# Kernel optimization log

Hardware: AMD Instinct MI355X
Metric: run time of the kernel (lower is better)

The kernel has to match this reference:

```python
import jax, jax.numpy as jnp
import numpy as np

PAD_IDX = 0
NEG = -1e9


def gru_step(h, x, Wih, Whh, bih, bhh):
    # PyTorch GRU cell. Wih: [3H, In], Whh: [3H, H]
    gi = x @ Wih.T + bih
    gh = h @ Whh.T + bhh
    H = h.shape[-1]
    i_r, i_z, i_n = gi[..., :H], gi[..., H:2 * H], gi[..., 2 * H:]
    h_r, h_z, h_n = gh[..., :H], gh[..., H:2 * H], gh[..., 2 * H:]
    r = jax.nn.sigmoid(i_r + h_r)
    z = jax.nn.sigmoid(i_z + h_z)
    n = jnp.tanh(i_n + r * h_n)
    return (1.0 - z) * n + z * h


def setup_inputs() -> dict:
    key = jax.random.key(0)
    V, E, H, C = 256, 512, 1024, 128
    NM, NT, NP = 8, 12, 8
    B, S, T = 256, 96, 40
    ks = iter(jax.random.split(key, 40))

    def p(shape, scale=0.05):
        return (jax.random.normal(next(ks), shape, dtype=jnp.float32) * scale)

    enc_emb = p((V, E)).at[PAD_IDX].set(0.0)
    dec_emb = p((V, E)).at[PAD_IDX].set(0.0)
    inp = dict(
        src=jax.random.randint(next(ks), (B, S), 0, V, dtype=jnp.int32),
        tgt=jax.random.randint(next(ks), (B, T), 0, V, dtype=jnp.int32),
        mode_idx=jax.random.randint(next(ks), (B,), 0, NM, dtype=jnp.int32),
        tense_idx=jax.random.randint(next(ks), (B,), 0, NT, dtype=jnp.int32),
        person_idx=jax.random.randint(next(ks), (B,), 0, NP, dtype=jnp.int32),
        enc_emb=enc_emb,
        enc_Wih_f=p((3 * H, E)), enc_Whh_f=p((3 * H, H)),
        enc_bih_f=p((3 * H,)), enc_bhh_f=p((3 * H,)),
        enc_Wih_b=p((3 * H, E)), enc_Whh_b=p((3 * H, H)),
        enc_bih_b=p((3 * H,)), enc_bhh_b=p((3 * H,)),
        Wa=p((H, 3 * H)),           # attn: Linear(2H + H -> H), no bias
        va=p((1, H)),               # v: Linear(H -> 1), no bias
        dec_emb=dec_emb,
        dec_Wih=p((3 * H, E + 2 * H)), dec_Whh=p((3 * H, H)),
        dec_bih=p((3 * H,)), dec_bhh=p((3 * H,)),
        Wfc=p((V, H + 2 * H + E)), bfc=p((V,)),
        mode_E=p((NM, C)).at[0].set(0.0),
        tense_E=p((NT, C)).at[0].set(0.0),
        person_E=p((NP, C)).at[0].set(0.0),
        Wbr=p((H, 2 * H + 3 * C)), bbr=p((H,)),
    )
    return inp


def reference(src, tgt, mode_idx, tense_idx, person_idx,
              enc_emb, enc_Wih_f, enc_Whh_f, enc_bih_f, enc_bhh_f,
              enc_Wih_b, enc_Whh_b, enc_bih_b, enc_bhh_b,
              Wa, va, dec_emb, dec_Wih, dec_Whh, dec_bih, dec_bhh,
              Wfc, bfc, mode_E, tense_E, person_E, Wbr, bbr):
    B, S = src.shape
    T = tgt.shape[1]
    H = dec_Whh.shape[1]

    # ---- Encoder: bidirectional GRU ----
    x = enc_emb[src]                       # [B,S,E]
    xs = jnp.swapaxes(x, 0, 1)             # [S,B,E]
    h0 = jnp.zeros((B, H), dtype=x.dtype)

    def fstep(h, xt):
        h2 = gru_step(h, xt, enc_Wih_f, enc_Whh_f, enc_bih_f, enc_bhh_f)
        return h2, h2

    def bstep(h, xt):
        h2 = gru_step(h, xt, enc_Wih_b, enc_Whh_b, enc_bih_b, enc_bhh_b)
        return h2, h2

    hf, outs_f = jax.lax.scan(fstep, h0, xs)
    hb, outs_b = jax.lax.scan(bstep, h0, xs[::-1])
    outs_b = outs_b[::-1]
    enc_out = jnp.swapaxes(jnp.concatenate([outs_f, outs_b], axis=-1), 0, 1)  # [B,S,2H]
    enc_hidden = jnp.concatenate([hf, hb], axis=-1)                           # [B,2H]

    # ---- Bridge init of decoder hidden ----
    cond = jnp.concatenate([enc_hidden, mode_E[mode_idx], tense_E[tense_idx],
                            person_E[person_idx]], axis=-1)
    dec_h0 = jnp.tanh(cond @ Wbr.T + bbr)  # [B,H]

    # ---- Attention precompute (linear is separable over the concat) ----
    Wa_h, Wa_e = Wa[:, :H], Wa[:, H:]
    enc_proj = jnp.einsum('bsd,hd->bsh', enc_out, Wa_e)  # [B,S,H]
    src_mask = (src != PAD_IDX)

    # ---- Decoder greedy loop (eval: no teacher forcing) ----
    def step(carry, _):
        h, tok = carry
        energy = jnp.tanh(h @ Wa_h.T[None] if False else jnp.tanh(0))  # placeholder
        energy = jnp.tanh((h @ Wa_h.T)[:, None, :] + enc_proj)          # [B,S,H]
        scores = jnp.einsum('bsh,h->bs', energy, va[0])
        scores = jnp.where(src_mask, scores, NEG)
        w = jax.nn.softmax(scores, axis=-1)
        ctx = jnp.einsum('bs,bsd->bd', w, enc_out)                      # [B,2H]
        emb = dec_emb[tok]                                              # [B,E]
        rnn_in = jnp.concatenate([emb, ctx], axis=-1)
        h2 = gru_step(h, rnn_in, dec_Wih, dec_Whh, dec_bih, dec_bhh)
        pred = jnp.concatenate([h2, ctx, emb], axis=-1) @ Wfc.T + bfc   # [B,V]
        tok2 = jnp.argmax(pred, axis=-1).astype(tok.dtype)
        return (h2, tok2), pred

    (_, _), preds = jax.lax.scan(step, (dec_h0, tgt[:, 0]), None, length=T - 1)
    return jnp.swapaxes(preds, 0, 1)  # [B, T-1, V]
```

## Files before the change

kernel.cpp:

```cpp
#include <hip/hip_runtime.h>
#include <hip/hip_fp16.h>
#include <cstdint>
#include <cstddef>

#define B_  256
#define S_  96
#define T_  40
#define V_  256
#define E_  512
#define H_  1024
#define C_  128

typedef __attribute__((ext_vector_type(8))) short s8v;
typedef __attribute__((ext_vector_type(4))) float f4v;
typedef _Float16 h8v __attribute__((ext_vector_type(8)));

__device__ __forceinline__ float sigmoidf_(float x) { return 1.0f / (1.0f + expf(-x)); }

__device__ __forceinline__ uint32_t cvtpk_bf16(float a, float b) {
  uint32_t r;
  asm("v_cvt_pk_bf16_f32 %0, %1, %2" : "=v"(r) : "v"(a), "v"(b));
  return r;
}

union U4 { uint32_t u[4]; s8v v; };

__device__ __forceinline__ void split8(const float4 a, const float4 b, s8v& hi, s8v& lo) {
  U4 H, L;
  H.u[0] = cvtpk_bf16(a.x, a.y);
  H.u[1] = cvtpk_bf16(a.z, a.w);
  H.u[2] = cvtpk_bf16(b.x, b.y);
  H.u[3] = cvtpk_bf16(b.z, b.w);
  const float r0 = a.x - __uint_as_float(H.u[0] << 16);
  const float r1 = a.y - __uint_as_float(H.u[0] & 0xffff0000u);
  const float r2 = a.z - __uint_as_float(H.u[1] << 16);
  const float r3 = a.w - __uint_as_float(H.u[1] & 0xffff0000u);
  const float r4 = b.x - __uint_as_float(H.u[2] << 16);
  const float r5 = b.y - __uint_as_float(H.u[2] & 0xffff0000u);
  const float r6 = b.z - __uint_as_float(H.u[3] << 16);
  const float r7 = b.w - __uint_as_float(H.u[3] & 0xffff0000u);
  L.u[0] = cvtpk_bf16(r0, r1);
  L.u[1] = cvtpk_bf16(r2, r3);
  L.u[2] = cvtpk_bf16(r4, r5);
  L.u[3] = cvtpk_bf16(r6, r7);
  hi = H.v; lo = L.v;
}

__global__ void wsplit_k(const float* __restrict__ Wf, const float* __restrict__ Wb,
                         short* __restrict__ hi, short* __restrict__ lo, int n)
{
  const int i = blockIdx.x * 256 + threadIdx.x;
  const float w = (i < n) ? Wf[i] : Wb[i - n];
  const uint32_t h = cvtpk_bf16(w, w) & 0xffffu;
  const float wh = __uint_as_float(h << 16);
  const uint32_t l = cvtpk_bf16(w - wh, w - wh) & 0xffffu;
  hi[i] = (short)h;
  lo[i] = (short)l;
}

__global__ void split_plane_k(const float* __restrict__ src, int ld_src, int col0,
                              short* __restrict__ hi, short* __restrict__ lo,
                              int ld_p, int pcol0, int total, int cols)
{
  const int i = blockIdx.x * 256 + threadIdx.x;
  if (i >= total) return;
  const int r = i / cols, c = i % cols;
  const float w = src[(size_t)r * ld_src + col0 + c];
  const uint32_t h = cvtpk_bf16(w, w) & 0xffffu;
  const float wh = __uint_as_float(h << 16);
  const uint32_t l = cvtpk_bf16(w - wh, w - wh) & 0xffffu;
  const size_t o = (size_t)r * ld_p + pcol0 + c;
  hi[o] = (short)h;
  lo[o] = (short)l;
}

__global__ void split_plane_h_k(const float* __restrict__ src, int ld_src, int col0,
                                __half* __restrict__ hi, __half* __restrict__ lo,
                                int ld_p, int total, int cols)
{
  const int i = blockIdx.x * 256 + threadIdx.x;
  if (i >= total) return;
  const int r = i / cols, c = i % cols;
  const float w = src[(size_t)r * ld_src + col0 + c];
  const __half h = __float2half(w);
  const __half l = __float2half(w - __half2float(h));
  const size_t o = (size_t)r * ld_p + c;
  hi[o] = h;
  lo[o] = l;
}

struct EM {
  const int* gidx; int goff0, goff1;
  const float* Gt0; const float* Gt1;
  const float* h0; const float* h1; int ldh;
  const short* whi; const short* wlo;
  const float* bih0; const float* bih1;
  const float* bhh0; const float* bhh1;
  float* d0; float* d1;
  __half* e0; __half* e1; int lde;
};

__global__ __launch_bounds__(256)
void enc_mfma_k(EM g)
{
  const int fid = (blockIdx.x & 7) * 64 + (blockIdx.x >> 3);
  const int m0 = (fid & 3) * 64;
  const int r2 = fid >> 2;
  const int dir = r2 & 1;
  const int q0 = (r2 >> 1) * 16;

  __shared__ int rows[64];
  const int tid = threadIdx.x;
  if (tid < 64)
    rows[tid] = g.gidx[(size_t)(m0 + tid) * S_ + (dir ? g.goff1 : g.goff0)];
  __syncthreads();

  const int w = tid >> 6, lane = tid & 63;
  const int arow = m0 + 16 * w + (lane & 15);
  const int kc = (lane >> 4) << 3;
  const float* hsrc = dir ? g.h1 : g.h0;
  const short* whi = g.whi + (size_t)dir * (3u * H_ * H_);
  const short* wlo = g.wlo + (size_t)dir * (3u * H_ * H_);
  const float* ap = hsrc + (size_t)arow * g.ldh;
  const int wrow = q0 + (lane & 15);

  f4v acc[3];
  acc[0] = f4v{0.f, 0.f, 0.f, 0.f};
  acc[1] = f4v{0.f, 0.f, 0.f, 0.f};
  acc[2] = f4v{0.f, 0.f, 0.f, 0.f};

  float4 a0 = *(const float4*)(ap + kc);
  float4 a1 = *(const float4*)(ap + kc + 4);
  s8v bh[3], bl[3];
#pragma unroll
  for (int g3 = 0; g3 < 3; ++g3) {
    const size_t wb = (size_t)(g3 * H_ + wrow) * H_ + kc;
    bh[g3] = *(const s8v*)(whi + wb);
    bl[g3] = *(const s8v*)(wlo + wb);
  }

  for (int kb = 0; kb < 1024; kb += 32) {
    float4 na0, na1;
    s8v nbh[3], nbl[3];
    if (kb + 32 < 1024) {
      na0 = *(const float4*)(ap + kb + 32 + kc);
      na1 = *(const float4*)(ap + kb + 32 + kc + 4);
#pragma unroll
      for (int g3 = 0; g3 < 3; ++g3) {
        const size_t wb = (size_t)(g3 * H_ + wrow) * H_ + kb + 32 + kc;
        nbh[g3] = *(const s8v*)(whi + wb);
        nbl[g3] = *(const s8v*)(wlo + wb);
      }
    }
    s8v ah, al;
    split8(a0, a1, ah, al);
#pragma unroll
    for (int g3 = 0; g3 < 3; ++g3) {
      acc[g3] = __builtin_amdgcn_mfma_f32_16x16x32_bf16(ah, bh[g3], acc[g3], 0, 0, 0);
      acc[g3] = __builtin_amdgcn_mfma_f32_16x16x32_bf16(al, bh[g3], acc[g3], 0, 0, 0);
      acc[g3] = __builtin_amdgcn_mfma_f32_16x16x32_bf16(ah, bl[g3], acc[g3], 0, 0, 0);
    }
    a0 = na0; a1 = na1;
#pragma unroll
    for (int g3 = 0; g3 < 3; ++g3) { bh[g3] = nbh[g3]; bl[g3] = nbl[g3]; }
  }

  const float* bih = dir ? g.bih1 : g.bih0;
  const float* bhh = dir ? g.bhh1 : g.bhh0;
  const float* Gt = dir ? g.Gt1 : g.Gt0;
  float* dst = dir ? g.d1 : g.d0;
  __half* edst = dir ? g.e1 : g.e0;
  const int col = q0 + (lane & 15);
  const float bir = bih[col], biz = bih[H_ + col], bin = bih[2 * H_ + col];
  const float bhr = bhh[col], bhz = bhh[H_ + col], bhn = bhh[2 * H_ + col];
#pragma unroll
  for (int r = 0; r < 4; ++r) {
    const int b = m0 + 16 * w + (lane >> 4) * 4 + r;
    const float* Gr = Gt + (size_t)rows[b - m0] * (3 * H_);
    const float hold = hsrc[(size_t)b * g.ldh + col];
    const float rr = sigmoidf_(acc[0][r] + Gr[col] + bir + bhr);
    const float zz = sigmoidf_(acc[1][r] + Gr[H_ + col] + biz + bhz);
    const float nn = tanhf(Gr[2 * H_ + col] + bin + rr * (acc[2][r] + bhn));
    const float hv = (1.f - zz) * nn + zz * hold;
    dst[(size_t)b * H_ + col] = hv;
    edst[(size_t)b * g.lde + col] = __float2half(hv);
  }
}

struct DM {
  const float* predin;
  const float* h;
  const int* tok;
  const float* Gd;
  const short* whi; const short* wlo;
  const float* bih; const float* bhh;
  float* d;
  float* predout;
};

__global__ __launch_bounds__(768)
void dec_mfma_k(DM g)
{
  const int fid = (blockIdx.x & 7) * 32 + (blockIdx.x >> 3);
  const int m0 = (fid & 3) * 64;
  const int q0 = (fid >> 2) * 16;
  const int tid = threadIdx.x;
  const int w = tid >> 6, lane = tid & 63;
  const int mg = w & 3;
  const int gate = w >> 2;

  __shared__ short sA[2][2][64][40];
  __shared__ float eacc[4][64][16];

  const int srow = tid >> 2;
  const int skq = (tid & 3) << 3;
  const float* actx = g.predin + (size_t)(m0 + srow) * 3584 + 1024;
  const float* ahid = g.h + (size_t)(m0 + srow) * H_;
  auto loadA8 = [&](int kk, float4& x0, float4& x1) {
    const float* p = (kk < 2048) ? (actx + kk) : (ahid + kk - 2048);
    x0 = *(const float4*)p;
    x1 = *(const float4*)(p + 4);
  };

  const int kc = (lane >> 4) << 3;
  const int wrow = gate * H_ + q0 + (lane & 15);
  const short* whp = g.whi + (size_t)wrow * 3072 + kc;
  const short* wlp = g.wlo + (size_t)wrow * 3072 + kc;

  f4v acc0 = f4v{0.f, 0.f, 0.f, 0.f};
  f4v acc1 = acc0;

  float4 sx0, sx1;
  if (tid < 256) loadA8(skq, sx0, sx1);
  s8v bh = *(const s8v*)whp;
  s8v bl = *(const s8v*)wlp;
  if (tid < 256) {
    s8v ah, al;
    split8(sx0, sx1, ah, al);
    *(s8v*)&sA[0][0][srow][skq] = ah;
    *(s8v*)&sA[0][1][srow][skq] = al;
  }
  __syncthreads();

  const int arowl = mg * 16 + (lane & 15);
  for (int ch = 0; ch < 96; ++ch) {
    const int buf = ch & 1;
    float4 nx0, nx1;
    if (tid < 256 && ch + 1 < 96) loadA8((ch + 1) * 32 + skq, nx0, nx1);
    s8v nbh, nbl;
    if (ch + 1 < 96) {
      nbh = *(const s8v*)(whp + (ch + 1) * 32);
      nbl = *(const s8v*)(wlp + (ch + 1) * 32);
    }
    const s8v ah = *(const s8v*)&sA[buf][0][arowl][kc];
    const s8v al = *(const s8v*)&sA[buf][1][arowl][kc];
    if (gate < 2) {
      acc0 = __builtin_amdgcn_mfma_f32_16x16x32_bf16(ah, bh, acc0, 0, 0, 0);
      acc0 = __builtin_amdgcn_mfma_f32_16x16x32_bf16(al, bh, acc0, 0, 0, 0);
      acc0 = __builtin_amdgcn_mfma_f32_16x16x32_bf16(ah, bl, acc0, 0, 0, 0);
    } else if (ch < 64) {
      acc0 = __builtin_amdgcn_mfma_f32_16x16x32_bf16(ah, bh, acc0, 0, 0, 0);
      acc0 = __builtin_amdgcn_mfma_f32_16x16x32_bf16(al, bh, acc0, 0, 0, 0);
      acc0 = __builtin_amdgcn_mfma_f32_16x16x32_bf16(ah, bl, acc0, 0, 0, 0);
    } else {
      acc1 = __builtin_amdgcn_mfma_f32_16x16x32_bf16(ah, bh, acc1, 0, 0, 0);
      acc1 = __builtin_amdgcn_mfma_f32_16x16x32_bf16(al, bh, acc1, 0, 0, 0);
      acc1 = __builtin_amdgcn_mfma_f32_16x16x32_bf16(ah, bl, acc1, 0, 0, 0);
    }
    if (tid < 256 && ch + 1 < 96) {
      s8v ah2, al2;
      split8(nx0, nx1, ah2, al2);
      *(s8v*)&sA[buf ^ 1][0][srow][skq] = ah2;
      *(s8v*)&sA[buf ^ 1][1][srow][skq] = al2;
    }
    bh = nbh; bl = nbl;
    __syncthreads();
  }

#pragma unroll
  for (int r = 0; r < 4; ++r) {
    const int lr = mg * 16 + (lane >> 4) * 4 + r;
    if (gate < 2) {
      eacc[gate][lr][lane & 15] = acc0[r];
    } else {
      eacc[2][lr][lane & 15] = acc0[r];
      eacc[3][lr][lane & 15] = acc1[r];
    }
  }
  __syncthreads();

  for (int o = tid; o < 1024; o += 768) {
    const int lr = o >> 4, lc = o & 15;
    const int b = m0 + lr, col = q0 + lc;
    const float* Gr = g.Gd + (size_t)g.tok[b] * (3 * H_);
    const float hold = g.h[(size_t)b * H_ + col];
    const float rr = sigmoidf_(eacc[0][lr][lc] + Gr[col] + g.bih[col] + g.bhh[col]);
    const float zz = sigmoidf_(eacc[1][lr][lc] + Gr[H_ + col] + g.bih[H_ + col] + g.bhh[H_ + col]);
    const float nn = tanhf(eacc[2][lr][lc] + Gr[2 * H_ + col] + g.bih[2 * H_ + col]
                           + rr * (eacc[3][lr][lc] + g.bhh[2 * H_ + col]));
    const float hv = (1.f - zz) * nn + zz * hold;
    g.d[(size_t)b * H_ + col] = hv;
    g.predout[(size_t)b * 3584 + col] = hv;
  }
}

__global__ __launch_bounds__(256)
void proj_mfma_k(const __half* __restrict__ enc, const __half* __restrict__ whi,
                 const __half* __restrict__ wlo, __half* __restrict__ proj)
{
  const int fid = (blockIdx.x & 7) * 768 + (blockIdx.x >> 3);
  const int w = threadIdx.x >> 6, lane = threadIdx.x & 63;
  const int wg = fid * 4 + w;
  const int ng = wg / 1536;
  const int mt = wg % 1536;
  const int n0 = ng * 64;
  const int kc = (lane >> 4) << 3;
  const __half* ap = enc + (size_t)(mt * 16 + (lane & 15)) * 2048 + kc;
  const __half* bhp = whi + (size_t)(n0 + (lane & 15)) * 2048 + kc;
  const __half* blp = wlo + (size_t)(n0 + (lane & 15)) * 2048 + kc;

  f4v acc[4];
#pragma unroll
  for (int j = 0; j < 4; ++j) acc[j] = f4v{0.f, 0.f, 0.f, 0.f};

  h8v a = *(const h8v*)ap;
  h8v bh[4], bl[4];
#pragma unroll
  for (int j = 0; j < 4; ++j) {
    bh[j] = *(const h8v*)(bhp + (size_t)j * 16 * 2048);
    bl[j] = *(const h8v*)(blp + (size_t)j * 16 * 2048);
  }

  for (int kb = 0; kb < 2048; kb += 32) {
    h8v na, nbh[4], nbl[4];
    if (kb + 32 < 2048) {
      na = *(const h8v*)(ap + kb + 32);
#pragma unroll
      for (int j = 0; j < 4; ++j) {
        nbh[j] = *(const h8v*)(bhp + (size_t)j * 16 * 2048 + kb + 32);
        nbl[j] = *(const h8v*)(blp + (size_t)j * 16 * 2048 + kb + 32);
      }
    }
#pragma unroll
    for (int j = 0; j < 4; ++j) {
      acc[j] = __builtin_amdgcn_mfma_f32_16x16x32_f16(a, bh[j], acc[j], 0, 0, 0);
      acc[j] = __builtin_amdgcn_mfma_f32_16x16x32_f16(a, bl[j], acc[j], 0, 0, 0);
    }
    a = na;
#pragma unroll
    for (int j = 0; j < 4; ++j) { bh[j] = nbh[j]; bl[j] = nbl[j]; }
  }

#pragma unroll
  for (int j = 0; j < 4; ++j)
#pragma unroll
    for (int r = 0; r < 4; ++r) {
      const int row = mt * 16 + (lane >> 4) * 4 + r;
      proj[(size_t)row * H_ + n0 + j * 16 + (lane & 15)] = __float2half(acc[j][r]);
    }
}

__global__ __launch_bounds__(256)
void prqa_mfma_k(const float* __restrict__ predin,
                 const short* __restrict__ fhi, const short* __restrict__ flo,
                 const float* __restrict__ bfc,
                 const float* __restrict__ hnew,
                 const short* __restrict__ qhi, const short* __restrict__ qlo,
                 float* __restrict__ out_t, float* __restrict__ qout)
{
  const int bid = blockIdx.x, tid = threadIdx.x;
  const int w = tid >> 6, lane = tid & 63;
  const int kc = (lane >> 4) << 3;
  if (bid < 256) {
    const int m0 = (bid >> 4) << 4, n0 = (bid & 15) << 4;
    const float* ap = predin + (size_t)(m0 + (lane & 15)) * 3584 + w * 896;
    const short* bhp = fhi + (size_t)(n0 + (lane & 15)) * 3584 + w * 896;
    const short* blp = flo + (size_t)(n0 + (lane & 15)) * 3584 + w * 896;
    f4v acc = f4v{0.f, 0.f, 0.f, 0.f};
    float4 a0 = *(const float4*)(ap + kc), a1 = *(const float4*)(ap + kc + 4);
    s8v bh = *(const s8v*)(bhp + kc), bl = *(const s8v*)(blp + kc);
    for (int kb = 0; kb < 896; kb += 32) {
      float4 na0, na1; s8v nbh, nbl;
      if (kb + 32 < 896) {
        na0 = *(const float4*)(ap + kb + 32 + kc);
        na1 = *(const float4*)(ap + kb + 32 + kc + 4);
        nbh = *(const s8v*)(bhp + kb + 32 + kc);
        nbl = *(const s8v*)(blp + kb + 32 + kc);
      }
      s8v ah, al;
      split8(a0, a1, ah, al);
      acc = __builtin_amdgcn_mfma_f32_16x16x32_bf16(ah, bh, acc, 0, 0, 0);
      acc = __builtin_amdgcn_mfma_f32_16x16x32_bf16(al, bh, acc, 0, 0, 0);
      acc = __builtin_amdgcn_mfma_f32_16x16x32_bf16(ah, bl, acc, 0, 0, 0);
      a0 = na0; a1 = na1; bh = nbh; bl = nbl;
    }
    __shared__ float red[4][64][4];
#pragma unroll
    for (int r = 0; r < 4; ++r) red[w][lane][r] = acc[r];
    __syncthreads();
    const int row = tid >> 4, col = tid & 15;
    const int sl = col + ((row >> 2) << 4), reg = row & 3;
    const float s = red[0][sl][reg] + red[1][sl][reg] + red[2][sl][reg] + red[3][sl][reg];
    out_t[(size_t)(m0 + row) * ((T_ - 1) * V_) + n0 + col] = s + bfc[n0 + col];
  } else {
    const int tt = (bid - 256) * 4 + w;
    const int m0 = (tt >> 6) << 4, n0 = (tt & 63) << 4;
    const float* ap = hnew + (size_t)(m0 + (lane & 15)) * H_;
    const short* bhp = qhi + (size_t)(n0 + (lane & 15)) * H_;
    const short* blp = qlo + (size_t)(n0 + (lane & 15)) * H_;
    f4v acc = f4v{0.f, 0.f, 0.f, 0.f};
    float4 a0 = *(const float4*)(ap + kc), a1 = *(const float4*)(ap + kc + 4);
    s8v bh = *(const s8v*)(bhp + kc), bl = *(const s8v*)(blp + kc);
    for (int kb = 0; kb < 1024; kb += 32) {
      float4 na0, na1; s8v nbh, nbl;
      if (kb + 32 < 1024) {
        na0 = *(const float4*)(ap + kb + 32 + kc);
        na1 = *(const float4*)(ap + kb + 32 + kc + 4);
        nbh = *(const s8v*)(bhp + kb + 32 + kc);
        nbl = *(const s8v*)(blp + kb + 32 + kc);
      }
      s8v ah, al;
      split8(a0, a1, ah, al);
      acc = __builtin_amdgcn_mfma_f32_16x16x32_bf16(ah, bh, acc, 0, 0, 0);
      acc = __builtin_amdgcn_mfma_f32_16x16x32_bf16(al, bh, acc, 0, 0, 0);
      acc = __builtin_amdgcn_mfma_f32_16x16x32_bf16(ah, bl, acc, 0, 0, 0);
      a0 = na0; a1 = na1; bh = nbh; bl = nbl;
    }
#pragma unroll
    for (int r = 0; r < 4; ++r)
      qout[(size_t)(m0 + (lane >> 4) * 4 + r) * H_ + n0 + (lane & 15)] = acc[r];
  }
}

__global__ __launch_bounds__(512)
void attn1_k(const float* __restrict__ out, const int* __restrict__ tgt,
             const float* __restrict__ q, const __half* __restrict__ proj,
             const float* __restrict__ va, const int* __restrict__ src,
             const float* __restrict__ dec_emb,
             float* __restrict__ predin, float* __restrict__ wts,
             int* __restrict__ tokbuf, int t)
{
  const int b = blockIdx.x, tid = threadIdx.x;
  const int lane = tid & 63, wv = tid >> 6;
  __shared__ float sm[128];
  __shared__ float tr[128];
  __shared__ float rv[4];
  __shared__ int ri[4];
  __shared__ int tok_s;
  if (t == 0) {
    if (tid == 0) tok_s = tgt[(size_t)b * T_];
  } else {
    if (tid < 256) {
      float av = out[((size_t)b * (T_ - 1) + (t - 1)) * V_ + tid];
      int ai = tid;
      for (int off = 32; off; off >>= 1) {
        const float ov = __shfl_down(av, off);
        const int   oi = __shfl_down(ai, off);
        if (ov > av) { av = ov; ai = oi; }
      }
      if (lane == 0) { rv[wv] = av; ri[wv] = ai; }
    }
    __syncthreads();
    if (tid == 0) {
      float bv = rv[0]; int bi = ri[0];
      for (int w2 = 1; w2 < 4; ++w2) if (rv[w2] > bv) { bv = rv[w2]; bi = ri[w2]; }
      tok_s = bi;
    }
  }
  __syncthreads();
  const int tok = tok_s;
  if (tid == 0) tokbuf[b] = tok;
  predin[(size_t)b * 3584 + 3072 + tid] = dec_emb[(size_t)tok * E_ + tid];
  const float* qb = q + (size_t)b * H_;
  for (int s = wv * 12; s < wv * 12 + 12; ++s) {
    const __half* pb = proj + ((size_t)b * S_ + s) * H_;
    float part = 0.f;
#pragma unroll
    for (int j = 0; j < 8; ++j) {
      const int h = lane * 2 + j * 128;
      const __half2 p2 = *(const __half2*)(pb + h);
      const float2 q2 = *(const float2*)(qb + h);
      const float2 v2 = *(const float2*)(va + h);
      part += v2.x * tanhf(q2.x + __half2float(p2.x));
      part += v2.y * tanhf(q2.y + __half2float(p2.y));
    }
    for (int off = 32; off; off >>= 1) part += __shfl_down(part, off);
    if (lane == 0)
      sm[s] = (src[(size_t)b * S_ + s] == 0) ? -1.0e9f : part;
  }
  __syncthreads();
  if (tid < 128) tr[tid] = (tid < S_) ? sm[tid] : -3.0e38f;
  __syncthreads();
  for (int s2 = 64; s2 > 0; s2 >>= 1) { if (tid < s2) tr[tid] = fmaxf(tr[tid], tr[tid + s2]); __syncthreads(); }
  const float mx = tr[0];
  __syncthreads();
  if (tid < 128) tr[tid] = (tid < S_) ? expf(sm[tid] - mx) : 0.f;
  __syncthreads();
  for (int s2 = 64; s2 > 0; s2 >>= 1) { if (tid < s2) tr[tid] += tr[tid + s2]; __syncthreads(); }
  const float inv = 1.0f / tr[0];
  __syncthreads();
  if (tid < S_) wts[(size_t)b * S_ + tid] = expf(sm[tid] - mx) * inv;
}

__global__ __launch_bounds__(256)
void ctx_k(const float* __restrict__ wts, const __half* __restrict__ enc,
           float* __restrict__ predin)
{
  const int b = blockIdx.y, tid = threadIdx.x;
  __shared__ float sw[S_];
  if (tid < S_) sw[tid] = wts[(size_t)b * S_ + tid];
  __syncthreads();
  const int d = blockIdx.x * 512 + tid * 2;
  const __half* eb = enc + (size_t)b * S_ * (2 * H_) + d;
  float c0 = 0.f, c1 = 0.f;
  for (int s0 = 0; s0 < S_; s0 += 8) {
    __half2 v[8];
#pragma unroll
    for (int i = 0; i < 8; ++i) v[i] = *(const __half2*)(eb + (size_t)(s0 + i) * (2 * H_));
#pragma unroll
    for (int i = 0; i < 8; ++i) {
      const float w = sw[s0 + i];
      c0 += w * __half2float(v[i].x);
      c1 += w * __half2float(v[i].y);
    }
  }
  *(float2*)(predin + (size_t)b * 3584 + H_ + d) = make_float2(c0, c1);
}

struct GB {
  const float* A; int lda;
  const __half* Ah;
  const float* W; int ldw;
  const float* bias;
  float* C; int ldc;
  __half* Ch;
  int M, N, K, act;
  const float *hf, *hb; int ldh;
  const float *mE, *tE, *pE;
  const int *mi, *ti, *pi;
};

template<int AMODE, int CMODE>
__global__ __launch_bounds__(256)
void gemm_k(GB g0, GB g1)
{
  GB g = blockIdx.z ? g1 : g0;
  const int m0 = blockIdx.y * 64, n0 = blockIdx.x * 64;
  if (m0 >= g.M || n0 >= g.N) return;
  __shared__ float As[32][68];
  __shared__ float Ws[32][68];
  const int tid = threadIdx.x, tx = tid & 15, ty = tid >> 4;
  const int lm = tid >> 3, lk = (tid & 7) << 2;
  float acc[4][4] = {};
  float4 av[2], wv[2], av2[2], wv2[2];

  auto load_tile = [&](int k0, float4 (&AV)[2], float4 (&WV)[2]) {
#pragma unroll
    for (int i = 0; i < 2; ++i) {
      const int row = lm + i * 32;
      const int kk = k0 + lk;
      if (AMODE == 0) {
        AV[i] = *(const float4*)(g.A + (size_t)(m0 + row) * g.lda + kk);
      } else if (AMODE == 4) {
        const __half* ap = g.Ah + (size_t)(m0 + row) * g.lda + kk;
        const __half2 h0 = *(const __half2*)ap;
        const __half2 h1 = *(const __half2*)(ap + 2);
        AV[i] = make_float4(__half2float(h0.x), __half2float(h0.y),
                            __half2float(h1.x), __half2float(h1.y));
      } else {
        const int mg = m0 + row; const float* sp; size_t o;
        if (kk < 1024)      { sp = g.hf; o = (size_t)mg * g.ldh + kk; }
        else if (kk < 2048) { sp = g.hb; o = (size_t)mg * g.ldh + kk - 1024; }
        else if (kk < 2176) { sp = g.mE; o = (size_t)g.mi[mg] * C_ + kk - 2048; }
        else if (kk < 2304) { sp = g.tE; o = (size_t)g.ti[mg] * C_ + kk - 2176; }
        else                { sp = g.pE; o = (size_t)g.pi[mg] * C_ + kk - 2304; }
        AV[i] = *(const float4*)(sp + o);
      }
      WV[i] = *(const float4*)(g.W + (size_t)(n0 + row) * g.ldw + kk);
    }
  };

  load_tile(0, av, wv);
  for (int k0 = 0; k0 < g.K; k0 += 32) {
    __syncthreads();
#pragma unroll
    for (int i = 0; i < 2; ++i) {
      const int row = lm + i * 32;
      As[lk + 0][row] = av[i].x; As[lk + 1][row] = av[i].y;
      As[lk + 2][row] = av[i].z; As[lk + 3][row] = av[i].w;
      Ws[lk + 0][row] = wv[i].x; Ws[lk + 1][row] = wv[i].y;
      Ws[lk + 2][row] = wv[i].z; Ws[lk + 3][row] = wv[i].w;
    }
    __syncthreads();
    if (k0 + 32 < g.K) load_tile(k0 + 32, av2, wv2);
#pragma unroll
    for (int k = 0; k < 32; ++k) {
      const float4 a4 = *(const float4*)&As[k][ty << 2];
      const float4 b4 = *(const float4*)&Ws[k][tx << 2];
      acc[0][0] += a4.x * b4.x; acc[0][1] += a4.x * b4.y; acc[0][2] += a4.x * b4.z; acc[0][3] += a4.x * b4.w;
      acc[1][0] += a4.y * b4.x; acc[1][1] += a4.y * b4.y; acc[1][2] += a4.y * b4.z; acc[1][3] += a4.y * b4.w;
      acc[2][0] += a4.z * b4.x; acc[2][1] += a4.z * b4.y; acc[2][2] += a4.z * b4.z; acc[2][3] += a4.z * b4.w;
      acc[3][0] += a4.w * b4.x; acc[3][1] += a4.w * b4.y; acc[3][2] += a4.w * b4.z; acc[3][3] += a4.w * b4.w;
    }
#pragma unroll
    for (int i = 0; i < 2; ++i) { av[i] = av2[i]; wv[i] = wv2[i]; }
  }
  const int n = n0 + (tx << 2);
  float4 bb = make_float4(0.f, 0.f, 0.f, 0.f);
  if (g.bias) bb = *(const float4*)(g.bias + n);
#pragma unroll
  for (int i = 0; i < 4; ++i) {
    const int m = m0 + (ty << 2) + i;
    float4 v = make_float4(acc[i][0] + bb.x, acc[i][1] + bb.y, acc[i][2] + bb.z, acc[i][3] + bb.w);
    if (CMODE == 0) {
      if (g.act) { v.x = tanhf(v.x); v.y = tanhf(v.y); v.z = tanhf(v.z); v.w = tanhf(v.w); }
      *(float4*)(g.C + (size_t)m * g.ldc + n) = v;
    } else {
      __half2* cp = (__half2*)(g.Ch + (size_t)m * g.ldc + n);
      cp[0] = __floats2half2_rn(v.x, v.y);
      cp[1] = __floats2half2_rn(v.z, v.w);
    }
  }
}

__global__ void zero_k(float* __restrict__ p, int n)
{
  const int i = blockIdx.x * 256 + threadIdx.x;
  if (i < n) p[i] = 0.0f;
}

__global__ void sentinel_k(float* out, float v) { out[threadIdx.x] = v; }

extern "C" void kernel_launch(void* const* d_in, const int* in_sizes, int n_in,
                              void* d_out, int out_size, void* d_ws, size_t ws_size,
                              hipStream_t stream)
{
  const int*   src        = (const int*)d_in[0];
  const int*   tgt        = (const int*)d_in[1];
  const int*   mode_idx   = (const int*)d_in[2];
  const int*   tense_idx  = (const int*)d_in[3];
  const int*   person_idx = (const int*)d_in[4];
  const float* enc_emb    = (const float*)d_in[5];
  const float* eWih_f     = (const float*)d_in[6];
  const float* eWhh_f     = (const float*)d_in[7];
  const float* ebih_f     = (const float*)d_in[8];
  const float* ebhh_f     = (const float*)d_in[9];
  const float* eWih_b     = (const float*)d_in[10];
  const float* eWhh_b     = (const float*)d_in[11];
  const float* ebih_b     = (const float*)d_in[12];
  const float* ebhh_b     = (const float*)d_in[13];
  const float* Wa         = (const float*)d_in[14];
  const float* va         = (const float*)d_in[15];
  const float* dec_emb    = (const float*)d_in[16];
  const float* dWih       = (const float*)d_in[17];
  const float* dWhh       = (const float*)d_in[18];
  const float* dbih       = (const float*)d_in[19];
  const float* dbhh       = (const float*)d_in[20];
  const float* Wfc        = (const float*)d_in[21];
  const float* bfc        = (const float*)d_in[22];
  const float* mode_E     = (const float*)d_in[23];
  const float* tense_E    = (const float*)d_in[24];
  const float* person_E   = (const float*)d_in[25];
  const float* Wbr        = (const float*)d_in[26];
  const float* bbr        = (const float*)d_in[27];
  float* out = (float*)d_out;

  char* base = (char*)d_ws;
  size_t off = 0;
  auto alloc = [&](size_t bytes) { char* r = base + off; off = (off + bytes + 255) & ~(size_t)255; return r; };
  __half* enc_out = (__half*)alloc(2ull * B_ * S_ * 2 * H_);
  __half* proj    = (__half*)alloc(2ull * B_ * S_ * H_);
  short* whh_hi = (short*)alloc(2ull * 2 * 3 * H_ * H_);
  short* whh_lo = (short*)alloc(2ull * 2 * 3 * H_ * H_);
  short* dpl_hi = (short*)alloc(2ull * 3 * H_ * 3072);
  short* dpl_lo = (short*)alloc(2ull * 3 * H_ * 3072);
  short* fc_hi  = (short*)alloc(2ull * V_ * 3584);
  short* fc_lo  = (short*)alloc(2ull * V_ * 3584);
  short* qa_hi  = (short*)alloc(2ull * H_ * H_);
  short* qa_lo  = (short*)alloc(2ull * H_ * H_);
  __half* wae_hi = (__half*)alloc(2ull * H_ * 2048);
  __half* wae_lo = (__half*)alloc(2ull * H_ * 2048);
  float* Gi_f  = (float*)alloc(4ull * V_ * 3 * H_);
  float* Gi_b  = (float*)alloc(4ull * V_ * 3 * H_);
  float* Gd    = (float*)alloc(4ull * V_ * 3 * H_);
  float* hfA   = (float*)alloc(4ull * B_ * H_);
  float* hfB   = (float*)alloc(4ull * B_ * H_);
  float* hbA   = (float*)alloc(4ull * B_ * H_);
  float* hbB   = (float*)alloc(4ull * B_ * H_);
  float* h_d0  = (float*)alloc(4ull * B_ * H_);
  float* h_d1  = (float*)alloc(4ull * B_ * H_);
  float* q     = (float*)alloc(4ull * B_ * H_);
  float* predin = (float*)alloc(4ull * B_ * 3584);
  float* wts   = (float*)alloc(4ull * B_ * S_);
  int*   tok   = (int*)alloc(4ull * B_);
  float* zero_buf = (float*)alloc(4ull * 1024);
  if (off > ws_size) {
    hipLaunchKernelGGL(sentinel_k, dim3(1), dim3(256), 0, stream, out,
                       1000.0f + (float)(ws_size >> 20));
    return;
  }

  hipLaunchKernelGGL(zero_k, dim3(4), dim3(256), 0, stream, zero_buf, 1024);

  {
    const int n = 3 * H_ * H_;
    hipLaunchKernelGGL(wsplit_k, dim3((2 * n) / 256), dim3(256), 0, stream,
                       eWhh_f, eWhh_b, whh_hi, whh_lo, n);
    int tot = 3 * H_ * 2048;
    hipLaunchKernelGGL(split_plane_k, dim3((tot + 255) / 256), dim3(256), 0, stream,
                       dWih, 2560, 512, dpl_hi, dpl_lo, 3072, 0, tot, 2048);
    tot = 3 * H_ * 1024;
    hipLaunchKernelGGL(split_plane_k, dim3((tot + 255) / 256), dim3(256), 0, stream,
                       dWhh, 1024, 0, dpl_hi, dpl_lo, 3072, 2048, tot, 1024);
    tot = V_ * 3584;
    hipLaunchKernelGGL(split_plane_k, dim3((tot + 255) / 256), dim3(256), 0, stream,
                       Wfc, 3584, 0, fc_hi, fc_lo, 3584, 0, tot, 3584);
    tot = H_ * 1024;
    hipLaunchKernelGGL(split_plane_k, dim3((tot + 255) / 256), dim3(256), 0, stream,
                       Wa, 3 * H_, 0, qa_hi, qa_lo, 1024, 0, tot, 1024);
    tot = H_ * 2048;
    hipLaunchKernelGGL(split_plane_h_k, dim3((tot + 255) / 256), dim3(256), 0, stream,
                       Wa, 3 * H_, 1024, wae_hi, wae_lo, 2048, tot, 2048);
  }

  GB Z{};

  {
    GB t0 = Z, t1 = Z;
    t0.A = enc_emb; t0.lda = E_; t0.W = eWih_f; t0.ldw = E_;
    t0.C = Gi_f; t0.ldc = 3 * H_; t0.M = V_; t0.N = 3 * H_; t0.K = E_;
    t1 = t0; t1.W = eWih_b; t1.C = Gi_b;
    hipLaunchKernelGGL((gemm_k<0, 0>), dim3(48, 4, 2), dim3(256), 0, stream, t0, t1);
    GB t2 = Z;
    t2.A = dec_emb; t2.lda = E_; t2.W = dWih; t2.ldw = 2560;
    t2.C = Gd; t2.ldc = 3 * H_; t2.M = V_; t2.N = 3 * H_; t2.K = E_;
    hipLaunchKernelGGL((gemm_k<0, 0>), dim3(48, 4, 1), dim3(256), 0, stream, t2, t2);
  }

  for (int t = 0; t < S_; ++t) {
    EM em{};
    em.gidx = src; em.goff0 = t; em.goff1 = S_ - 1 - t;
    em.Gt0 = Gi_f; em.Gt1 = Gi_b;
    if (t == 0) { em.h0 = zero_buf; em.h1 = zero_buf; em.ldh = 0; }
    else if (t & 1) { em.h0 = hfA; em.h1 = hbA; em.ldh = H_; }
    else            { em.h0 = hfB; em.h1 = hbB; em.ldh = H_; }
    em.whi = whh_hi; em.wlo = whh_lo;
    em.bih0 = ebih_f; em.bih1 = ebih_b; em.bhh0 = ebhh_f; em.bhh1 = ebhh_b;
    if (t & 1) { em.d0 = hfB; em.d1 = hbB; } else { em.d0 = hfA; em.d1 = hbA; }
    em.e0 = enc_out + (size_t)t * 2 * H_;
    em.e1 = enc_out + (size_t)(S_ - 1 - t) * 2 * H_ + H_;
    em.lde = S_ * 2 * H_;
    hipLaunchKernelGGL(enc_mfma_k, dim3(512), dim3(256), 0, stream, em);
  }
  float* hf_fin = hfB;
  float* hb_fin = hbB;

  hipLaunchKernelGGL(proj_mfma_k, dim3(6144), dim3(256), 0, stream,
                     enc_out, wae_hi, wae_lo, proj);

  {
    GB br = Z;
    br.W = Wbr; br.ldw = 2432; br.bias = bbr; br.C = h_d0; br.ldc = H_;
    br.M = B_; br.N = H_; br.K = 2432; br.act = 1;
    br.hf = hf_fin; br.hb = hb_fin; br.ldh = H_;
    br.mE = mode_E; br.tE = tense_E; br.pE = person_E;
    br.mi = mode_idx; br.ti = tense_idx; br.pi = person_idx;
    hipLaunchKernelGGL((gemm_k<2, 0>), dim3(16, 4, 1), dim3(256), 0, stream, br, br);
  }

  {
    GB qa = Z;
    qa.A = h_d0; qa.lda = H_; qa.W = Wa; qa.ldw = 3 * H_; qa.C = q; qa.ldc = H_;
    qa.M = B_; qa.N = H_; qa.K = H_;
    hipLaunchKernelGGL((gemm_k<0, 0>), dim3(16, 4, 1), dim3(256), 0, stream, qa, qa);
  }

  float* hd[2] = { h_d0, h_d1 };
  for (int t = 0; t < T_ - 1; ++t) {
    hipLaunchKernelGGL(attn1_k, dim3(B_), dim3(512), 0, stream,
                       out, tgt, q, proj, va, src, dec_emb, predin, wts, tok, t);
    hipLaunchKernelGGL(ctx_k, dim3(4, B_), dim3(256), 0, stream, wts, enc_out, predin);

    DM dm{};
    dm.predin = predin;
    dm.h = hd[t & 1];
    dm.tok = tok; dm.Gd = Gd;
    dm.whi = dpl_hi; dm.wlo = dpl_lo;
    dm.bih = dbih; dm.bhh = dbhh;
    dm.d = hd[(t + 1) & 1];
    dm.predout = predin;
    hipLaunchKernelGGL(dec_mfma_k, dim3(256), dim3(768), 0, stream, dm);

    hipLaunchKernelGGL(prqa_mfma_k, dim3(512), dim3(256), 0, stream,
                       predin, fc_hi, fc_lo, bfc, hd[(t + 1) & 1], qa_hi, qa_lo,
                       out + (size_t)t * V_, q);
  }
}
```

Before: 14.27 ms.

## Store activations as pre-split bf16 hi/lo planes at producer

```diff
diff --git a/kernel.cpp b/kernel.cpp
--- a/kernel.cpp
+++ b/kernel.cpp
@@ -23,27 +23,11 @@
   return r;
 }
 
-union U4 { uint32_t u[4]; s8v v; };
-
-__device__ __forceinline__ void split8(const float4 a, const float4 b, s8v& hi, s8v& lo) {
-  U4 H, L;
-  H.u[0] = cvtpk_bf16(a.x, a.y);
-  H.u[1] = cvtpk_bf16(a.z, a.w);
-  H.u[2] = cvtpk_bf16(b.x, b.y);
-  H.u[3] = cvtpk_bf16(b.z, b.w);
-  const float r0 = a.x - __uint_as_float(H.u[0] << 16);
-  const float r1 = a.y - __uint_as_float(H.u[0] & 0xffff0000u);
-  const float r2 = a.z - __uint_as_float(H.u[1] << 16);
-  const float r3 = a.w - __uint_as_float(H.u[1] & 0xffff0000u);
-  const float r4 = b.x - __uint_as_float(H.u[2] << 16);
-  const float r5 = b.y - __uint_as_float(H.u[2] & 0xffff0000u);
-  const float r6 = b.z - __uint_as_float(H.u[3] << 16);
-  const float r7 = b.w - __uint_as_float(H.u[3] & 0xffff0000u);
-  L.u[0] = cvtpk_bf16(r0, r1);
-  L.u[1] = cvtpk_bf16(r2, r3);
-  L.u[2] = cvtpk_bf16(r4, r5);
-  L.u[3] = cvtpk_bf16(r6, r7);
-  hi = H.v; lo = L.v;
+__device__ __forceinline__ void split1(float v, short& hi, short& lo) {
+  const uint32_t h = cvtpk_bf16(v, v) & 0xffffu;
+  const float hf = __uint_as_float(h << 16);
+  const uint32_t l = cvtpk_bf16(v - hf, v - hf) & 0xffffu;
+  hi = (short)h; lo = (short)l;
 }
 
 __global__ void wsplit_k(const float* __restrict__ Wf, const float* __restrict__ Wb,
@@ -51,11 +35,8 @@
 {
   const int i = blockIdx.x * 256 + threadIdx.x;
   const float w = (i < n) ? Wf[i] : Wb[i - n];
-  const uint32_t h = cvtpk_bf16(w, w) & 0xffffu;
-  const float wh = __uint_as_float(h << 16);
-  const uint32_t l = cvtpk_bf16(w - wh, w - wh) & 0xffffu;
-  hi[i] = (short)h;
-  lo[i] = (short)l;
+  short h, l; split1(w, h, l);
+  hi[i] = h; lo[i] = l;
 }
 
 __global__ void split_plane_k(const float* __restrict__ src, int ld_src, int col0,
@@ -65,13 +46,9 @@
   const int i = blockIdx.x * 256 + threadIdx.x;
   if (i >= total) return;
   const int r = i / cols, c = i % cols;
-  const float w = src[(size_t)r * ld_src + col0 + c];
-  const uint32_t h = cvtpk_bf16(w, w) & 0xffffu;
-  const float wh = __uint_as_float(h << 16);
-  const uint32_t l = cvtpk_bf16(w - wh, w - wh) & 0xffffu;
+  short h, l; split1(src[(size_t)r * ld_src + col0 + c], h, l);
   const size_t o = (size_t)r * ld_p + pcol0 + c;
-  hi[o] = (short)h;
-  lo[o] = (short)l;
+  hi[o] = h; lo[o] = l;
 }
 
 __global__ void split_plane_h_k(const float* __restrict__ src, int ld_src, int col0,
@@ -85,18 +62,29 @@
   const __half h = __float2half(w);
   const __half l = __float2half(w - __half2float(h));
   const size_t o = (size_t)r * ld_p + c;
-  hi[o] = h;
-  lo[o] = l;
+  hi[o] = h; lo[o] = l;
+}
+
+__global__ void h0split_k(const float* __restrict__ h, short* __restrict__ phi,
+                          short* __restrict__ plo)
+{
+  const int i = blockIdx.x * 256 + threadIdx.x;
+  short hh, ll; split1(h[i], hh, ll);
+  phi[i] = hh;
+  plo[i] = ll;
 }
 
 struct EM {
   const int* gidx; int goff0, goff1;
   const float* Gt0; const float* Gt1;
-  const float* h0; const float* h1; int ldh;
+  const float* h0f; const float* h1f; int ldh;
+  const short* ah0; const short* al0;
+  const short* ah1; const short* al1;
   const short* whi; const short* wlo;
   const float* bih0; const float* bih1;
   const float* bhh0; const float* bhh1;
   float* d0; float* d1;
+  short* dh0; short* dl0; short* dh1; short* dl1;
   __half* e0; __half* e1; int lde;
 };
 
@@ -118,19 +106,18 @@
   const int w = tid >> 6, lane = tid & 63;
   const int arow = m0 + 16 * w + (lane & 15);
   const int kc = (lane >> 4) << 3;
-  const float* hsrc = dir ? g.h1 : g.h0;
+  const short* aph = (dir ? g.ah1 : g.ah0) + (size_t)arow * H_;
+  const short* apl = (dir ? g.al1 : g.al0) + (size_t)arow * H_;
   const short* whi = g.whi + (size_t)dir * (3u * H_ * H_);
   const short* wlo = g.wlo + (size_t)dir * (3u * H_ * H_);
-  const float* ap = hsrc + (size_t)arow * g.ldh;
   const int wrow = q0 + (lane & 15);
 
   f4v acc[3];
   acc[0] = f4v{0.f, 0.f, 0.f, 0.f};
-  acc[1] = f4v{0.f, 0.f, 0.f, 0.f};
-  acc[2] = f4v{0.f, 0.f, 0.f, 0.f};
-
-  float4 a0 = *(const float4*)(ap + kc);
-  float4 a1 = *(const float4*)(ap + kc + 4);
+  acc[1] = acc[0]; acc[2] = acc[0];
+
+  s8v ah = *(const s8v*)(aph + kc);
+  s8v al = *(const s8v*)(apl + kc);
   s8v bh[3], bl[3];
 #pragma unroll
   for (int g3 = 0; g3 < 3; ++g3) {
@@ -140,11 +127,10 @@
   }
 
   for (int kb = 0; kb < 1024; kb += 32) {
-    float4 na0, na1;
-    s8v nbh[3], nbl[3];
+    s8v nah, nal, nbh[3], nbl[3];
     if (kb + 32 < 1024) {
-      na0 = *(const float4*)(ap + kb + 32 + kc);
-      na1 = *(const float4*)(ap + kb + 32 + kc + 4);
+      nah = *(const s8v*)(aph + kb + 32 + kc);
+      nal = *(const s8v*)(apl + kb + 32 + kc);
 #pragma unroll
       for (int g3 = 0; g3 < 3; ++g3) {
         const size_t wb = (size_t)(g3 * H_ + wrow) * H_ + kb + 32 + kc;
@@ -152,15 +138,13 @@
         nbl[g3] = *(const s8v*)(wlo + wb);
       }
     }
-    s8v ah, al;
-    split8(a0, a1, ah, al);
 #pragma unroll
     for (int g3 = 0; g3 < 3; ++g3) {
       acc[g3] = __builtin_amdgcn_mfma_f32_16x16x32_bf16(ah, bh[g3], acc[g3], 0, 0, 0);
       acc[g3] = __builtin_amdgcn_mfma_f32_16x16x32_bf16(al, bh[g3], acc[g3], 0, 0, 0);
       acc[g3] = __builtin_amdgcn_mfma_f32_16x16x32_bf16(ah, bl[g3], acc[g3], 0, 0, 0);
     }
-    a0 = na0; a1 = na1;
+    ah = nah; al = nal;
 #pragma unroll
     for (int g3 = 0; g3 < 3; ++g3) { bh[g3] = nbh[g3]; bl[g3] = nbl[g3]; }
   }
@@ -168,7 +152,10 @@
   const float* bih = dir ? g.bih1 : g.bih0;
   const float* bhh = dir ? g.bhh1 : g.bhh0;
   const float* Gt = dir ? g.Gt1 : g.Gt0;
+  const float* hsrc = dir ? g.h1f : g.h0f;
   float* dst = dir ? g.d1 : g.d0;
+  short* dph = dir ? g.dh1 : g.dh0;
+  short* dpl = dir ? g.dl1 : g.dl0;
   __half* edst = dir ? g.e1 : g.e0;
   const int col = q0 + (lane & 15);
   const float bir = bih[col], biz = bih[H_ + col], bin = bih[2 * H_ + col];
@@ -183,19 +170,23 @@
     const float nn = tanhf(Gr[2 * H_ + col] + bin + rr * (acc[2][r] + bhn));
     const float hv = (1.f - zz) * nn + zz * hold;
     dst[(size_t)b * H_ + col] = hv;
+    short hh, ll; split1(hv, hh, ll);
+    dph[(size_t)b * H_ + col] = hh;
+    dpl[(size_t)b * H_ + col] = ll;
     edst[(size_t)b * g.lde + col] = __float2half(hv);
   }
 }
 
 struct DM {
-  const float* predin;
+  const short* phi; const short* plo;
+  const short* hhi; const short* hlo;
   const float* h;
   const int* tok;
   const float* Gd;
   const short* whi; const short* wlo;
   const float* bih; const float* bhh;
   float* d;
-  float* predout;
+  short* dhhi; short* dhlo;
 };
 
 __global__ __launch_bounds__(768)
@@ -209,20 +200,14 @@
   const int mg = w & 3;
   const int gate = w >> 2;
 
-  __shared__ short sA[2][2][64][40];
   __shared__ float eacc[4][64][16];
 
-  const int srow = tid >> 2;
-  const int skq = (tid & 3) << 3;
-  const float* actx = g.predin + (size_t)(m0 + srow) * 3584 + 1024;
-  const float* ahid = g.h + (size_t)(m0 + srow) * H_;
-  auto loadA8 = [&](int kk, float4& x0, float4& x1) {
-    const float* p = (kk < 2048) ? (actx + kk) : (ahid + kk - 2048);
-    x0 = *(const float4*)p;
-    x1 = *(const float4*)(p + 4);
-  };
-
   const int kc = (lane >> 4) << 3;
+  const int arow = m0 + mg * 16 + (lane & 15);
+  const short* aph = g.phi + (size_t)arow * 3584;
+  const short* apl = g.plo + (size_t)arow * 3584;
+  const short* ahh = g.hhi + (size_t)arow * H_;
+  const short* ahl = g.hlo + (size_t)arow * H_;
   const int wrow = gate * H_ + q0 + (lane & 15);
   const short* whp = g.whi + (size_t)wrow * 3072 + kc;
   const short* wlp = g.wlo + (size_t)wrow * 3072 + kc;
@@ -230,51 +215,33 @@
   f4v acc0 = f4v{0.f, 0.f, 0.f, 0.f};
   f4v acc1 = acc0;
 
-  float4 sx0, sx1;
-  if (tid < 256) loadA8(skq, sx0, sx1);
+  auto aload = [&](int kk, s8v& hh, s8v& ll) {
+    if (kk < 2048) {
+      hh = *(const s8v*)(aph + 1024 + kk);
+      ll = *(const s8v*)(apl + 1024 + kk);
+    } else {
+      hh = *(const s8v*)(ahh + kk - 2048);
+      ll = *(const s8v*)(ahl + kk - 2048);
+    }
+  };
+
+  s8v ah, al;
+  aload(kc, ah, al);
   s8v bh = *(const s8v*)whp;
   s8v bl = *(const s8v*)wlp;
-  if (tid < 256) {
-    s8v ah, al;
-    split8(sx0, sx1, ah, al);
-    *(s8v*)&sA[0][0][srow][skq] = ah;
-    *(s8v*)&sA[0][1][srow][skq] = al;
-  }
-  __syncthreads();
-
-  const int arowl = mg * 16 + (lane & 15);
+
   for (int ch = 0; ch < 96; ++ch) {
-    const int buf = ch & 1;
-    float4 nx0, nx1;
-    if (tid < 256 && ch + 1 < 96) loadA8((ch + 1) * 32 + skq, nx0, nx1);
-    s8v nbh, nbl;
+    s8v nah, nal, nbh, nbl;
     if (ch + 1 < 96) {
+      aload((ch + 1) * 32 + kc, nah, nal);
       nbh = *(const s8v*)(whp + (ch + 1) * 32);
       nbl = *(const s8v*)(wlp + (ch + 1) * 32);
     }
-    const s8v ah = *(const s8v*)&sA[buf][0][arowl][kc];
-    const s8v al = *(const s8v*)&sA[buf][1][arowl][kc];
-    if (gate < 2) {
-      acc0 = __builtin_amdgcn_mfma_f32_16x16x32_bf16(ah, bh, acc0, 0, 0, 0);
-      acc0 = __builtin_amdgcn_mfma_f32_16x16x32_bf16(al, bh, acc0, 0, 0, 0);
-      acc0 = __builtin_amdgcn_mfma_f32_16x16x32_bf16(ah, bl, acc0, 0, 0, 0);
-    } else if (ch < 64) {
-      acc0 = __builtin_amdgcn_mfma_f32_16x16x32_bf16(ah, bh, acc0, 0, 0, 0);
-      acc0 = __builtin_amdgcn_mfma_f32_16x16x32_bf16(al, bh, acc0, 0, 0, 0);
-      acc0 = __builtin_amdgcn_mfma_f32_16x16x32_bf16(ah, bl, acc0, 0, 0, 0);
-    } else {
-      acc1 = __builtin_amdgcn_mfma_f32_16x16x32_bf16(ah, bh, acc1, 0, 0, 0);
-      acc1 = __builtin_amdgcn_mfma_f32_16x16x32_bf16(al, bh, acc1, 0, 0, 0);
-      acc1 = __builtin_amdgcn_mfma_f32_16x16x32_bf16(ah, bl, acc1, 0, 0, 0);
-    }
-    if (tid < 256 && ch + 1 < 96) {
-      s8v ah2, al2;
-      split8(nx0, nx1, ah2, al2);
-      *(s8v*)&sA[buf ^ 1][0][srow][skq] = ah2;
-      *(s8v*)&sA[buf ^ 1][1][srow][skq] = al2;
-    }
-    bh = nbh; bl = nbl;
-    __syncthreads();
+    f4v& a = (gate < 2 || ch < 64) ? acc0 : acc1;
+    a = __builtin_amdgcn_mfma_f32_16x16x32_bf16(ah, bh, a, 0, 0, 0);
+    a = __builtin_amdgcn_mfma_f32_16x16x32_bf16(al, bh, a, 0, 0, 0);
+    a = __builtin_amdgcn_mfma_f32_16x16x32_bf16(ah, bl, a, 0, 0, 0);
+    ah = nah; al = nal; bh = nbh; bl = nbl;
   }
 
 #pragma unroll
@@ -300,7 +267,9 @@
                            + rr * (eacc[3][lr][lc] + g.bhh[2 * H_ + col]));
     const float hv = (1.f - zz) * nn + zz * hold;
     g.d[(size_t)b * H_ + col] = hv;
-    g.predout[(size_t)b * 3584 + col] = hv;
+    short hh, ll; split1(hv, hh, ll);
+    g.dhhi[(size_t)b * H_ + col] = hh;
+    g.dhlo[(size_t)b * H_ + col] = ll;
   }
 }
 
@@ -361,10 +330,10 @@
 }
 
 __global__ __launch_bounds__(256)
-void prqa_mfma_k(const float* __restrict__ predin,
+void prqa_mfma_k(const short* __restrict__ phi, const short* __restrict__ plo,
+                 const short* __restrict__ hn_hi, const short* __restrict__ hn_lo,
                  const short* __restrict__ fhi, const short* __restrict__ flo,
                  const float* __restrict__ bfc,
-                 const float* __restrict__ hnew,
                  const short* __restrict__ qhi, const short* __restrict__ qlo,
                  float* __restrict__ out_t, float* __restrict__ qout)
 {
@@ -373,26 +342,34 @@
   const int kc = (lane >> 4) << 3;
   if (bid < 256) {
     const int m0 = (bid >> 4) << 4, n0 = (bid & 15) << 4;
-    const float* ap = predin + (size_t)(m0 + (lane & 15)) * 3584 + w * 896;
+    const int arow = m0 + (lane & 15);
     const short* bhp = fhi + (size_t)(n0 + (lane & 15)) * 3584 + w * 896;
     const short* blp = flo + (size_t)(n0 + (lane & 15)) * 3584 + w * 896;
+    auto aload = [&](int kb, s8v& hh, s8v& ll) {
+      const int gk = w * 896 + kb;
+      if (gk < 1024) {
+        hh = *(const s8v*)(hn_hi + (size_t)arow * H_ + gk);
+        ll = *(const s8v*)(hn_lo + (size_t)arow * H_ + gk);
+      } else {
+        hh = *(const s8v*)(phi + (size_t)arow * 3584 + gk);
+        ll = *(const s8v*)(plo + (size_t)arow * 3584 + gk);
+      }
+    };
     f4v acc = f4v{0.f, 0.f, 0.f, 0.f};
-    float4 a0 = *(const float4*)(ap + kc), a1 = *(const float4*)(ap + kc + 4);
+    s8v ah, al;
+    aload(kc, ah, al);
     s8v bh = *(const s8v*)(bhp + kc), bl = *(const s8v*)(blp + kc);
     for (int kb = 0; kb < 896; kb += 32) {
-      float4 na0, na1; s8v nbh, nbl;
+      s8v nah, nal, nbh, nbl;
       if (kb + 32 < 896) {
-        na0 = *(const float4*)(ap + kb + 32 + kc);
-        na1 = *(const float4*)(ap + kb + 32 + kc + 4);
+        aload(kb + 32 + kc, nah, nal);
         nbh = *(const s8v*)(bhp + kb + 32 + kc);
         nbl = *(const s8v*)(blp + kb + 32 + kc);
       }
-      s8v ah, al;
-      split8(a0, a1, ah, al);
       acc = __builtin_amdgcn_mfma_f32_16x16x32_bf16(ah, bh, acc, 0, 0, 0);
       acc = __builtin_amdgcn_mfma_f32_16x16x32_bf16(al, bh, acc, 0, 0, 0);
       acc = __builtin_amdgcn_mfma_f32_16x16x32_bf16(ah, bl, acc, 0, 0, 0);
-      a0 = na0; a1 = na1; bh = nbh; bl = nbl;
+      ah = nah; al = nal; bh = nbh; bl = nbl;
     }
     __shared__ float red[4][64][4];
 #pragma unroll
@@ -405,26 +382,25 @@
   } else {
     const int tt = (bid - 256) * 4 + w;
     const int m0 = (tt >> 6) << 4, n0 = (tt & 63) << 4;
-    const float* ap = hnew + (size_t)(m0 + (lane & 15)) * H_;
+    const short* aph = hn_hi + (size_t)(m0 + (lane & 15)) * H_;
+    const short* apl = hn_lo + (size_t)(m0 + (lane & 15)) * H_;
     const short* bhp = qhi + (size_t)(n0 + (lane & 15)) * H_;
     const short* blp = qlo + (size_t)(n0 + (lane & 15)) * H_;
     f4v acc = f4v{0.f, 0.f, 0.f, 0.f};
-    float4 a0 = *(const float4*)(ap + kc), a1 = *(const float4*)(ap + kc + 4);
+    s8v ah = *(const s8v*)(aph + kc), al = *(const s8v*)(apl + kc);
     s8v bh = *(const s8v*)(bhp + kc), bl = *(const s8v*)(blp + kc);
     for (int kb = 0; kb < 1024; kb += 32) {
-      float4 na0, na1; s8v nbh, nbl;
+      s8v nah, nal, nbh, nbl;
       if (kb + 32 < 1024) {
-        na0 = *(const float4*)(ap + kb + 32 + kc);
-        na1 = *(const float4*)(ap + kb + 32 + kc + 4);
+        nah = *(const s8v*)(aph + kb + 32 + kc);
+        nal = *(const s8v*)(apl + kb + 32 + kc);
         nbh = *(const s8v*)(bhp + kb + 32 + kc);
         nbl = *(const s8v*)(blp + kb + 32 + kc);
       }
-      s8v ah, al;
-      split8(a0, a1, ah, al);
       acc = __builtin_amdgcn_mfma_f32_16x16x32_bf16(ah, bh, acc, 0, 0, 0);
       acc = __builtin_amdgcn_mfma_f32_16x16x32_bf16(al, bh, acc, 0, 0, 0);
       acc = __builtin_amdgcn_mfma_f32_16x16x32_bf16(ah, bl, acc, 0, 0, 0);
-      a0 = na0; a1 = na1; bh = nbh; bl = nbl;
+      ah = nah; al = nal; bh = nbh; bl = nbl;
     }
 #pragma unroll
     for (int r = 0; r < 4; ++r)
@@ -437,8 +413,8 @@
              const float* __restrict__ q, const __half* __restrict__ proj,
              const float* __restrict__ va, const int* __restrict__ src,
              const float* __restrict__ dec_emb,
-             float* __restrict__ predin, float* __restrict__ wts,
-             int* __restrict__ tokbuf, int t)
+             short* __restrict__ phi, short* __restrict__ plo,
+             float* __restrict__ wts, int* __restrict__ tokbuf, int t)
 {
   const int b = blockIdx.x, tid = threadIdx.x;
   const int lane = tid & 63, wv = tid >> 6;
@@ -470,7 +446,11 @@
   __syncthreads();
   const int tok = tok_s;
   if (tid == 0) tokbuf[b] = tok;
-  predin[(size_t)b * 3584 + 3072 + tid] = dec_emb[(size_t)tok * E_ + tid];
+  {
+    short hh, ll; split1(dec_emb[(size_t)tok * E_ + tid], hh, ll);
+    phi[(size_t)b * 3584 + 3072 + tid] = hh;
+    plo[(size_t)b * 3584 + 3072 + tid] = ll;
+  }
   const float* qb = q + (size_t)b * H_;
   for (int s = wv * 12; s < wv * 12 + 12; ++s) {
     const __half* pb = proj + ((size_t)b * S_ + s) * H_;
@@ -504,7 +484,7 @@
 
 __global__ __launch_bounds__(256)
 void ctx_k(const float* __restrict__ wts, const __half* __restrict__ enc,
-           float* __restrict__ predin)
+           short* __restrict__ phi, short* __restrict__ plo)
 {
   const int b = blockIdx.y, tid = threadIdx.x;
   __shared__ float sw[S_];
@@ -524,23 +504,26 @@
       c1 += w * __half2float(v[i].y);
     }
   }
-  *(float2*)(predin + (size_t)b * 3584 + H_ + d) = make_float2(c0, c1);
+  short h0, l0, h1, l1;
+  split1(c0, h0, l0);
+  split1(c1, h1, l1);
+  const size_t o = (size_t)b * 3584 + 1024 + d;
+  phi[o] = h0; phi[o + 1] = h1;
+  plo[o] = l0; plo[o + 1] = l1;
 }
 
 struct GB {
   const float* A; int lda;
-  const __half* Ah;
   const float* W; int ldw;
   const float* bias;
   float* C; int ldc;
-  __half* Ch;
   int M, N, K, act;
   const float *hf, *hb; int ldh;
   const float *mE, *tE, *pE;
   const int *mi, *ti, *pi;
 };
 
-template<int AMODE, int CMODE>
+template<int AMODE>
 __global__ __launch_bounds__(256)
 void gemm_k(GB g0, GB g1)
 {
@@ -561,12 +544,6 @@
       const int kk = k0 + lk;
       if (AMODE == 0) {
         AV[i] = *(const float4*)(g.A + (size_t)(m0 + row) * g.lda + kk);
-      } else if (AMODE == 4) {
-        const __half* ap = g.Ah + (size_t)(m0 + row) * g.lda + kk;
-        const __half2 h0 = *(const __half2*)ap;
-        const __half2 h1 = *(const __half2*)(ap + 2);
-        AV[i] = make_float4(__half2float(h0.x), __half2float(h0.y),
-                            __half2float(h1.x), __half2float(h1.y));
       } else {
         const int mg = m0 + row; const float* sp; size_t o;
         if (kk < 1024)      { sp = g.hf; o = (size_t)mg * g.ldh + kk; }
@@ -612,14 +589,8 @@
   for (int i = 0; i < 4; ++i) {
     const int m = m0 + (ty << 2) + i;
     float4 v = make_float4(acc[i][0] + bb.x, acc[i][1] + bb.y, acc[i][2] + bb.z, acc[i][3] + bb.w);
-    if (CMODE == 0) {
-      if (g.act) { v.x = tanhf(v.x); v.y = tanhf(v.y); v.z = tanhf(v.z); v.w = tanhf(v.w); }
-      *(float4*)(g.C + (size_t)m * g.ldc + n) = v;
-    } else {
-      __half2* cp = (__half2*)(g.Ch + (size_t)m * g.ldc + n);
-      cp[0] = __floats2half2_rn(v.x, v.y);
-      cp[1] = __floats2half2_rn(v.z, v.w);
-    }
+    if (g.act) { v.x = tanhf(v.x); v.y = tanhf(v.y); v.z = tanhf(v.z); v.w = tanhf(v.w); }
+    *(float4*)(g.C + (size_t)m * g.ldc + n) = v;
   }
 }
 
@@ -687,13 +658,27 @@
   float* hfB   = (float*)alloc(4ull * B_ * H_);
   float* hbA   = (float*)alloc(4ull * B_ * H_);
   float* hbB   = (float*)alloc(4ull * B_ * H_);
+  short* hpfA_hi = (short*)alloc(2ull * B_ * H_);
+  short* hpfA_lo = (short*)alloc(2ull * B_ * H_);
+  short* hpfB_hi = (short*)alloc(2ull * B_ * H_);
+  short* hpfB_lo = (short*)alloc(2ull * B_ * H_);
+  short* hpbA_hi = (short*)alloc(2ull * B_ * H_);
+  short* hpbA_lo = (short*)alloc(2ull * B_ * H_);
+  short* hpbB_hi = (short*)alloc(2ull * B_ * H_);
+  short* hpbB_lo = (short*)alloc(2ull * B_ * H_);
   float* h_d0  = (float*)alloc(4ull * B_ * H_);
   float* h_d1  = (float*)alloc(4ull * B_ * H_);
+  short* hp0_hi = (short*)alloc(2ull * B_ * H_);
+  short* hp0_lo = (short*)alloc(2ull * B_ * H_);
+  short* hp1_hi = (short*)alloc(2ull * B_ * H_);
+  short* hp1_lo = (short*)alloc(2ull * B_ * H_);
   float* q     = (float*)alloc(4ull * B_ * H_);
-  float* predin = (float*)alloc(4ull * B_ * 3584);
+  short* pin_hi = (short*)alloc(2ull * B_ * 3584);
+  short* pin_lo = (short*)alloc(2ull * B_ * 3584);
   float* wts   = (float*)alloc(4ull * B_ * S_);
   int*   tok   = (int*)alloc(4ull * B_);
   float* zero_buf = (float*)alloc(4ull * 1024);
+  short* zero_pl  = (short*)alloc(2ull * B_ * H_);
   if (off > ws_size) {
     hipLaunchKernelGGL(sentinel_k, dim3(1), dim3(256), 0, stream, out,
                        1000.0f + (float)(ws_size >> 20));
@@ -701,6 +686,8 @@
   }
 
   hipLaunchKernelGGL(zero_k, dim3(4), dim3(256), 0, stream, zero_buf, 1024);
+  hipLaunchKernelGGL(zero_k, dim3((B_ * H_ / 2) / 256), dim3(256), 0, stream,
+                     (float*)zero_pl, B_ * H_ / 2);
 
   {
     const int n = 3 * H_ * H_;
@@ -730,23 +717,36 @@
     t0.A = enc_emb; t0.lda = E_; t0.W = eWih_f; t0.ldw = E_;
     t0.C = Gi_f; t0.ldc = 3 * H_; t0.M = V_; t0.N = 3 * H_; t0.K = E_;
     t1 = t0; t1.W = eWih_b; t1.C = Gi_b;
-    hipLaunchKernelGGL((gemm_k<0, 0>), dim3(48, 4, 2), dim3(256), 0, stream, t0, t1);
+    hipLaunchKernelGGL((gemm_k<0>), dim3(48, 4, 2), dim3(256), 0, stream, t0, t1);
     GB t2 = Z;
     t2.A = dec_emb; t2.lda = E_; t2.W = dWih; t2.ldw = 2560;
     t2.C = Gd; t2.ldc = 3 * H_; t2.M = V_; t2.N = 3 * H_; t2.K = E_;
-    hipLaunchKernelGGL((gemm_k<0, 0>), dim3(48, 4, 1), dim3(256), 0, stream, t2, t2);
+    hipLaunchKernelGGL((gemm_k<0>), dim3(48, 4, 1), dim3(256), 0, stream, t2, t2);
   }
 
   for (int t = 0; t < S_; ++t) {
     EM em{};
     em.gidx = src; em.goff0 = t; em.goff1 = S_ - 1 - t;
     em.Gt0 = Gi_f; em.Gt1 = Gi_b;
-    if (t == 0) { em.h0 = zero_buf; em.h1 = zero_buf; em.ldh = 0; }
-    else if (t & 1) { em.h0 = hfA; em.h1 = hbA; em.ldh = H_; }
-    else            { em.h0 = hfB; em.h1 = hbB; em.ldh = H_; }
+    if (t == 0) {
+      em.h0f = zero_buf; em.h1f = zero_buf; em.ldh = 0;
+      em.ah0 = zero_pl; em.al0 = zero_pl; em.ah1 = zero_pl; em.al1 = zero_pl;
+    } else if (t & 1) {
+      em.h0f = hfA; em.h1f = hbA; em.ldh = H_;
+      em.ah0 = hpfA_hi; em.al0 = hpfA_lo; em.ah1 = hpbA_hi; em.al1 = hpbA_lo;
+    } else {
+      em.h0f = hfB; em.h1f = hbB; em.ldh = H_;
+      em.ah0 = hpfB_hi; em.al0 = hpfB_lo; em.ah1 = hpbB_hi; em.al1 = hpbB_lo;
+    }
     em.whi = whh_hi; em.wlo = whh_lo;
     em.bih0 = ebih_f; em.bih1 = ebih_b; em.bhh0 = ebhh_f; em.bhh1 = ebhh_b;
-    if (t & 1) { em.d0 = hfB; em.d1 = hbB; } else { em.d0 = hfA; em.d1 = hbA; }
+    if (t & 1) {
+      em.d0 = hfB; em.d1 = hbB;
+      em.dh0 = hpfB_hi; em.dl0 = hpfB_lo; em.dh1 = hpbB_hi; em.dl1 = hpbB_lo;
+    } else {
+      em.d0 = hfA; em.d1 = hbA;
+      em.dh0 = hpfA_hi; em.dl0 = hpfA_lo; em.dh1 = hpbA_hi; em.dl1 = hpbA_lo;
+    }
     em.e0 = enc_out + (size_t)t * 2 * H_;
     em.e1 = enc_out + (size_t)(S_ - 1 - t) * 2 * H_ + H_;
     em.lde = S_ * 2 * H_;
@@ -765,34 +765,40 @@
     br.hf = hf_fin; br.hb = hb_fin; br.ldh = H_;
     br.mE = mode_E; br.tE = tense_E; br.pE = person_E;
     br.mi = mode_idx; br.ti = tense_idx; br.pi = person_idx;
-    hipLaunchKernelGGL((gemm_k<2, 0>), dim3(16, 4, 1), dim3(256), 0, stream, br, br);
-  }
+    hipLaunchKernelGGL((gemm_k<2>), dim3(16, 4, 1), dim3(256), 0, stream, br, br);
+  }
+  hipLaunchKernelGGL(h0split_k, dim3((B_ * H_) / 256), dim3(256), 0, stream,
+                     h_d0, hp0_hi, hp0_lo);
 
   {
     GB qa = Z;
     qa.A = h_d0; qa.lda = H_; qa.W = Wa; qa.ldw = 3 * H_; qa.C = q; qa.ldc = H_;
     qa.M = B_; qa.N = H_; qa.K = H_;
-    hipLaunchKernelGGL((gemm_k<0, 0>), dim3(16, 4, 1), dim3(256), 0, stream, qa, qa);
+    hipLaunchKernelGGL((gemm_k<0>), dim3(16, 4, 1), dim3(256), 0, stream, qa, qa);
   }
 
   float* hd[2] = { h_d0, h_d1 };
+  short* hphi[2] = { hp0_hi, hp1_hi };
+  short* hplo[2] = { hp0_lo, hp1_lo };
   for (int t = 0; t < T_ - 1; ++t) {
     hipLaunchKernelGGL(attn1_k, dim3(B_), dim3(512), 0, stream,
-                       out, tgt, q, proj, va, src, dec_emb, predin, wts, tok, t);
-    hipLaunchKernelGGL(ctx_k, dim3(4, B_), dim3(256), 0, stream, wts, enc_out, predin);
+                       out, tgt, q, proj, va, src, dec_emb, pin_hi, pin_lo, wts, tok, t);
+    hipLaunchKernelGGL(ctx_k, dim3(4, B_), dim3(256), 0, stream, wts, enc_out, pin_hi, pin_lo);
 
     DM dm{};
-    dm.predin = predin;
+    dm.phi = pin_hi; dm.plo = pin_lo;
+    dm.hhi = hphi[t & 1]; dm.hlo = hplo[t & 1];
     dm.h = hd[t & 1];
     dm.tok = tok; dm.Gd = Gd;
     dm.whi = dpl_hi; dm.wlo = dpl_lo;
     dm.bih = dbih; dm.bhh = dbhh;
     dm.d = hd[(t + 1) & 1];
-    dm.predout = predin;
+    dm.dhhi = hphi[(t + 1) & 1]; dm.dhlo = hplo[(t + 1) & 1];
     hipLaunchKernelGGL(dec_mfma_k, dim3(256), dim3(768), 0, stream, dm);
 
     hipLaunchKernelGGL(prqa_mfma_k, dim3(512), dim3(256), 0, stream,
-                       predin, fc_hi, fc_lo, bfc, hd[(t + 1) & 1], qa_hi, qa_lo,
+                       pin_hi, pin_lo, hphi[(t + 1) & 1], hplo[(t + 1) & 1],
+                       fc_hi, fc_lo, bfc, qa_hi, qa_lo,
                        out + (size_t)t * V_, q);
   }
 }
```

Measured after the change: 16.52 ms. 15.7% more time.
